# Kernel tuning notes

Measured on AMD Instinct MI355X. Metric: run time of the kernel, lower is better.

## Reference

```python
import jax, jax.numpy as jnp
import numpy as np

B, T, D, H = 2048, 2048, 3, 32  # batch, time steps, input_size, hidden_size


def setup_inputs() -> dict:
    key = jax.random.key(0)
    k0, k1, k2, k3, k4 = jax.random.split(key, 5)
    lim = 1.0 / np.sqrt(H)  # eqx.nn.GRUCell init range
    inp = jax.random.normal(k0, (B, T, D), dtype=jnp.float32)
    weight_ih = jax.random.uniform(k1, (3 * H, D), minval=-lim, maxval=lim, dtype=jnp.float32)
    weight_hh = jax.random.uniform(k2, (3 * H, H), minval=-lim, maxval=lim, dtype=jnp.float32)
    bias = jax.random.uniform(k3, (3 * H,), minval=-lim, maxval=lim, dtype=jnp.float32)
    bias_n = jax.random.uniform(k4, (H,), minval=-lim, maxval=lim, dtype=jnp.float32)
    return {"inp": inp, "weight_ih": weight_ih, "weight_hh": weight_hh,
            "bias": bias, "bias_n": bias_n}


def reference(inp, weight_ih, weight_hh, bias, bias_n):
    # inp: [B, T, D]. Faithful batched version of PinnWithGRU.__call__:
    # scan an eqx.nn.GRUCell over time from a zero hidden state, output hidden[0] per step.
    b = inp.shape[0]
    h0 = jnp.zeros((b, H), dtype=inp.dtype)
    xs = jnp.swapaxes(inp, 0, 1)  # [T, B, D]

    def step(h, x):
        ig = x @ weight_ih.T + bias      # [B, 3H] input gates (+ bias, as in eqx)
        hg = h @ weight_hh.T             # [B, 3H] hidden gates
        ir, iz, ia = jnp.split(ig, 3, axis=-1)
        hr, hz, ha = jnp.split(hg, 3, axis=-1)
        r = jax.nn.sigmoid(ir + hr)
        z = jax.nn.sigmoid(iz + hz)
        n = jnp.tanh(ia + bias_n + r * ha)
        h_new = (1.0 - z) * n + z * h
        return h_new, h_new[:, 0]        # emit first hidden unit per step

    _, out = jax.lax.scan(step, h0, xs)  # out: [T, B]
    return jnp.swapaxes(out, 0, 1)[..., None]  # [B, T, 1] (matches per-seq [T, 1])
```

## Files before the change

kernel.cpp:

```cpp
#include <hip/hip_runtime.h>


#define GRU_B 2048
#define GRU_T 2048
#define GRU_D 3
#define GRU_H 32
#define CHUNK 32

typedef unsigned int uint2v __attribute__((ext_vector_type(2)));

__device__ __forceinline__ float fast_sigmoid(float x) {
    float e = __expf(-x);
    return __builtin_amdgcn_rcpf(1.0f + e);
}
__device__ __forceinline__ float fast_tanh(float x) {
    float e = __expf(2.0f * x);
    return 1.0f - 2.0f * __builtin_amdgcn_rcpf(e + 1.0f);
}

#define DPPF(v, CTRL) __int_as_float(__builtin_amdgcn_update_dpp( \
    0, __float_as_int(v), (CTRL), 0xF, 0xF, false))

template<bool SEL>
__device__ __forceinline__ float swap32(float v) {
    uint2v r = __builtin_amdgcn_permlane32_swap(
        __float_as_uint(v), __float_as_uint(v), false, false);
    return __uint_as_float(SEL ? r.x : r.y);
}

template<bool SEL>
__device__ void gru_fast(
    const float* __restrict__ xp, float* __restrict__ ob,
    const float* __restrict__ w_ih, const float* __restrict__ w_hh,
    const float* __restrict__ bias, const float* __restrict__ bias_n,
    float* __restrict__ x_lds, float* __restrict__ out_stage,
    int lane, int hf, int p, int dir)
{
    const int li = lane & 15;
    const int bb = 16 * (lane >> 5);

    float wrO[16], wrX[16], wzO[16], wzX[16], wnO[16], wnX[16];
#pragma unroll
    for (int j = 0; j < 16; ++j) {
        const int kk = (li + dir * j + 16) & 15;
        const int kown = bb + kk;
        const int koth = (bb ^ 16) + kk;
        wrO[j] = w_hh[(size_t)p * GRU_H + kown];
        wrX[j] = w_hh[(size_t)p * GRU_H + koth];
        wzO[j] = w_hh[(size_t)(GRU_H + p) * GRU_H + kown];
        wzX[j] = w_hh[(size_t)(GRU_H + p) * GRU_H + koth];
        wnO[j] = w_hh[(size_t)(2 * GRU_H + p) * GRU_H + kown];
        wnX[j] = w_hh[(size_t)(2 * GRU_H + p) * GRU_H + koth];
    }
    float wir[GRU_D], wiz[GRU_D], win[GRU_D];
#pragma unroll
    for (int d = 0; d < GRU_D; ++d) {
        wir[d] = w_ih[(size_t)p * GRU_D + d];
        wiz[d] = w_ih[(size_t)(GRU_H + p) * GRU_D + d];
        win[d] = w_ih[(size_t)(2 * GRU_H + p) * GRU_D + d];
    }
    const float bR = bias[p];
    const float bZ = bias[GRU_H + p];
    const float bN = bias[2 * GRU_H + p] + bias_n[p];

    float* xw = x_lds + 96 * hf;
    const float* xr = x_lds + 96 * hf;
    float* osw = out_stage + 32 * hf;
    const bool cap = (lane & 47) == 0;

    float h = 0.0f;
    float xa = xp[p], xb = xp[32 + p], xc = xp[64 + p];

    for (int c = 0; c < GRU_T / CHUNK; ++c) {
        xw[p] = xa; xw[32 + p] = xb; xw[64 + p] = xc;
        if (c + 1 < GRU_T / CHUNK) {
            const size_t nb = (size_t)(c + 1) * (CHUNK * GRU_D);
            xa = xp[nb + p]; xb = xp[nb + 32 + p]; xc = xp[nb + 64 + p];
        }
#pragma unroll 8
        for (int s = 0; s < CHUNK; ++s) {
            const float x0 = xr[3 * s + 0];
            const float x1 = xr[3 * s + 1];
            const float x2 = xr[3 * s + 2];

            float hr_[16];
            hr_[0] = h;
            hr_[1]  = DPPF(h, 0x121); hr_[2]  = DPPF(h, 0x122);
            hr_[3]  = DPPF(h, 0x123); hr_[4]  = DPPF(h, 0x124);
            hr_[5]  = DPPF(h, 0x125); hr_[6]  = DPPF(h, 0x126);
            hr_[7]  = DPPF(h, 0x127); hr_[8]  = DPPF(h, 0x128);
            hr_[9]  = DPPF(h, 0x129); hr_[10] = DPPF(h, 0x12A);
            hr_[11] = DPPF(h, 0x12B); hr_[12] = DPPF(h, 0x12C);
            hr_[13] = DPPF(h, 0x12D); hr_[14] = DPPF(h, 0x12E);
            hr_[15] = DPPF(h, 0x12F);
            float ho_[16];
#pragma unroll
            for (int j = 0; j < 16; ++j) ho_[j] = swap32<SEL>(hr_[j]);

            const float aR = fmaf(wir[2], x2, fmaf(wir[1], x1, fmaf(wir[0], x0, bR)));
            const float aZ = fmaf(wiz[2], x2, fmaf(wiz[1], x1, fmaf(wiz[0], x0, bZ)));
            const float aN = fmaf(win[2], x2, fmaf(win[1], x1, fmaf(win[0], x0, bN)));

            float r0 = aR, r1 = 0.f, z0 = aZ, z1 = 0.f, n0 = 0.f, n1 = 0.f;
#pragma unroll
            for (int j = 0; j < 16; ++j) {
                r0 = fmaf(wrO[j], hr_[j], r0);
                r1 = fmaf(wrX[j], ho_[j], r1);
                z0 = fmaf(wzO[j], hr_[j], z0);
                z1 = fmaf(wzX[j], ho_[j], z1);
                n0 = fmaf(wnO[j], hr_[j], n0);
                n1 = fmaf(wnX[j], ho_[j], n1);
            }
            const float rg = fast_sigmoid(r0 + r1);
            const float zg = fast_sigmoid(z0 + z1);
            const float ng = fast_tanh(fmaf(rg, n0 + n1, aN));
            h = fmaf(zg, h - ng, ng);

            if (cap) osw[s] = h;
        }
        const float ov = osw[p];
        ob[c * CHUNK + p] = ov;
    }
}

__device__ void gru_lds(
    const float* __restrict__ xp, float* __restrict__ ob,
    const float* __restrict__ w_ih, const float* __restrict__ w_hh,
    const float* __restrict__ bias, const float* __restrict__ bias_n,
    float* __restrict__ x_lds, float* __restrict__ out_stage,
    float* __restrict__ h2, int lane, int hf, int p)
{
    float wr[32], wz[32], wn[32];
#pragma unroll
    for (int k = 0; k < 32; ++k) {
        wr[k] = w_hh[(size_t)p * GRU_H + k];
        wz[k] = w_hh[(size_t)(GRU_H + p) * GRU_H + k];
        wn[k] = w_hh[(size_t)(2 * GRU_H + p) * GRU_H + k];
    }
    float wir[GRU_D], wiz[GRU_D], win[GRU_D];
#pragma unroll
    for (int d = 0; d < GRU_D; ++d) {
        wir[d] = w_ih[(size_t)p * GRU_D + d];
        wiz[d] = w_ih[(size_t)(GRU_H + p) * GRU_D + d];
        win[d] = w_ih[(size_t)(2 * GRU_H + p) * GRU_D + d];
    }
    const float bR = bias[p];
    const float bZ = bias[GRU_H + p];
    const float bN = bias[2 * GRU_H + p] + bias_n[p];

    float* hw = h2 + 48 * hf + p;
    const float4* hv = (const float4*)(h2 + 48 * hf);
    float* xw = x_lds + 96 * hf;
    const float* xr = x_lds + 96 * hf;
    float* osw = out_stage + 32 * hf;
    const bool cap = (lane & 47) == 0;

    float h = 0.0f;
    *hw = 0.0f;
    float xa = xp[p], xb = xp[32 + p], xc = xp[64 + p];

    for (int c = 0; c < GRU_T / CHUNK; ++c) {
        xw[p] = xa; xw[32 + p] = xb; xw[64 + p] = xc;
        if (c + 1 < GRU_T / CHUNK) {
            const size_t nb = (size_t)(c + 1) * (CHUNK * GRU_D);
            xa = xp[nb + p]; xb = xp[nb + 32 + p]; xc = xp[nb + 64 + p];
        }
#pragma unroll 8
        for (int s = 0; s < CHUNK; ++s) {
            const float x0 = xr[3 * s + 0];
            const float x1 = xr[3 * s + 1];
            const float x2 = xr[3 * s + 2];
            float4 hk[8];
#pragma unroll
            for (int q = 0; q < 8; ++q) hk[q] = hv[q];

            const float aR = fmaf(wir[2], x2, fmaf(wir[1], x1, fmaf(wir[0], x0, bR)));
            const float aZ = fmaf(wiz[2], x2, fmaf(wiz[1], x1, fmaf(wiz[0], x0, bZ)));
            const float aN = fmaf(win[2], x2, fmaf(win[1], x1, fmaf(win[0], x0, bN)));

            float r0 = aR, r1 = 0.f, z0 = aZ, z1 = 0.f, n0 = 0.f, n1 = 0.f;
#pragma unroll
            for (int q = 0; q < 8; ++q) {
                const float4 v = hk[q];
                r0 = fmaf(wr[4*q+0], v.x, r0); r1 = fmaf(wr[4*q+1], v.y, r1);
                r0 = fmaf(wr[4*q+2], v.z, r0); r1 = fmaf(wr[4*q+3], v.w, r1);
                z0 = fmaf(wz[4*q+0], v.x, z0); z1 = fmaf(wz[4*q+1], v.y, z1);
                z0 = fmaf(wz[4*q+2], v.z, z0); z1 = fmaf(wz[4*q+3], v.w, z1);
                n0 = fmaf(wn[4*q+0], v.x, n0); n1 = fmaf(wn[4*q+1], v.y, n1);
                n0 = fmaf(wn[4*q+2], v.z, n0); n1 = fmaf(wn[4*q+3], v.w, n1);
            }
            const float rg = fast_sigmoid(r0 + r1);
            const float zg = fast_sigmoid(z0 + z1);
            const float ng = fast_tanh(fmaf(rg, n0 + n1, aN));
            h = fmaf(zg, h - ng, ng);
            if (cap) osw[s] = h;
            *hw = h;
        }
        const float ov = osw[p];
        ob[c * CHUNK + p] = ov;
    }
}

__global__ __launch_bounds__(64, 1) void gru_scan_kernel(
    const float* __restrict__ inp, const float* __restrict__ w_ih,
    const float* __restrict__ w_hh, const float* __restrict__ bias,
    const float* __restrict__ bias_n, float* __restrict__ out)
{
    __shared__ __align__(16) float x_lds[2 * CHUNK * GRU_D];
    __shared__ __align__(16) float out_stage[2 * CHUNK];
    __shared__ __align__(16) float h2[80];

    const int lane = threadIdx.x;
    const int hf   = (lane >> 4) & 1;
    const int p    = (lane & 15) + 16 * (lane >> 5);
    const size_t seq = 2 * (size_t)blockIdx.x + hf;

    const float* xp = inp + seq * (size_t)(GRU_T * GRU_D);
    float*       ob = out + seq * (size_t)GRU_T;

    int dir = 0;
    bool swapok = false, sel = false;
    {
        const int li = lane & 15;
        const int d1 = __builtin_amdgcn_update_dpp(0, li, 0x121, 0xF, 0xF, false);
        if (__ballot(d1 == ((li + 1) & 15)) == ~0ULL)       dir = 1;
        else if (__ballot(d1 == ((li + 15) & 15)) == ~0ULL) dir = -1;

        const unsigned ul = (unsigned)lane;
        uint2v q = __builtin_amdgcn_permlane32_swap(ul, ul, false, false);
        const unsigned want = ul ^ 32u;
        const bool okA = __ballot(q.x == want) == ~0ULL;
        const bool okB = __ballot(q.y == want) == ~0ULL;
        swapok = okA || okB;
        sel = okA;
    }

    if (dir != 0 && swapok) {
        if (sel) gru_fast<true >(xp, ob, w_ih, w_hh, bias, bias_n,
                                 x_lds, out_stage, lane, hf, p, dir);
        else     gru_fast<false>(xp, ob, w_ih, w_hh, bias, bias_n,
                                 x_lds, out_stage, lane, hf, p, dir);
    } else {
        gru_lds(xp, ob, w_ih, w_hh, bias, bias_n,
                x_lds, out_stage, h2, lane, hf, p);
    }
}

extern "C" void kernel_launch(void* const* d_in, const int* in_sizes, int n_in,
                              void* d_out, int out_size, void* d_ws, size_t ws_size,
                              hipStream_t stream) {
    const float* inp    = (const float*)d_in[0];
    const float* w_ih   = (const float*)d_in[1];
    const float* w_hh   = (const float*)d_in[2];
    const float* bias   = (const float*)d_in[3];
    const float* bias_n = (const float*)d_in[4];
    float* out = (float*)d_out;

    dim3 grid(GRU_B / 2);
    dim3 block(64);
    gru_scan_kernel<<<grid, block, 0, stream>>>(inp, w_ih, w_hh, bias, bias_n, out);
}
```

Before: 612.8 us.

## Cut per-step cross-lane ops and LDS traffic in the fast GRU recurrence

Swaps h across the 32-lane halves once with permlane32_swap and then applies the DPP rotations to both copies, which drops the 16 per-step swaps to one. Output capture moves from an LDS staging buffer to readlane/readfirstlane plus a per-lane register select. Next-step x values are prefetched from LDS one step ahead, the FMA accumulators are split into 12 shorter chains to shorten the dependency path, and the x tile is padded. The catch is twice as many DPP ops per step and two extra scalar readlanes on every step.

Result: no change. 601.2 us (-1.9%).

```diff
diff --git a/kernel.cpp b/kernel.cpp
--- a/kernel.cpp
+++ b/kernel.cpp
@@ -6,6 +6,7 @@
 #define GRU_D 3
 #define GRU_H 32
 #define CHUNK 32
+#define XPAD 104
 
 typedef unsigned int uint2v __attribute__((ext_vector_type(2)));
 
@@ -33,8 +34,7 @@
     const float* __restrict__ xp, float* __restrict__ ob,
     const float* __restrict__ w_ih, const float* __restrict__ w_hh,
     const float* __restrict__ bias, const float* __restrict__ bias_n,
-    float* __restrict__ x_lds, float* __restrict__ out_stage,
-    int lane, int hf, int p, int dir)
+    float* __restrict__ x_lds, int lane, int hf, int p, int dir)
 {
     const int li = lane & 15;
     const int bb = 16 * (lane >> 5);
@@ -63,10 +63,8 @@
     const float bZ = bias[GRU_H + p];
     const float bN = bias[2 * GRU_H + p] + bias_n[p];
 
-    float* xw = x_lds + 96 * hf;
-    const float* xr = x_lds + 96 * hf;
-    float* osw = out_stage + 32 * hf;
-    const bool cap = (lane & 47) == 0;
+    float* xw = x_lds + XPAD * hf;
+    const float* xr = x_lds + XPAD * hf;
 
     float h = 0.0f;
     float xa = xp[p], xb = xp[32 + p], xc = xp[64 + p];
@@ -77,49 +75,78 @@
             const size_t nb = (size_t)(c + 1) * (CHUNK * GRU_D);
             xa = xp[nb + p]; xb = xp[nb + 32 + p]; xc = xp[nb + 64 + p];
         }
+        float x0c = xr[0], x1c = xr[1], x2c = xr[2];
+        float outreg = 0.0f;
+
 #pragma unroll 8
         for (int s = 0; s < CHUNK; ++s) {
-            const float x0 = xr[3 * s + 0];
-            const float x1 = xr[3 * s + 1];
-            const float x2 = xr[3 * s + 2];
-
-            float hr_[16];
-            hr_[0] = h;
-            hr_[1]  = DPPF(h, 0x121); hr_[2]  = DPPF(h, 0x122);
-            hr_[3]  = DPPF(h, 0x123); hr_[4]  = DPPF(h, 0x124);
-            hr_[5]  = DPPF(h, 0x125); hr_[6]  = DPPF(h, 0x126);
-            hr_[7]  = DPPF(h, 0x127); hr_[8]  = DPPF(h, 0x128);
-            hr_[9]  = DPPF(h, 0x129); hr_[10] = DPPF(h, 0x12A);
-            hr_[11] = DPPF(h, 0x12B); hr_[12] = DPPF(h, 0x12C);
-            hr_[13] = DPPF(h, 0x12D); hr_[14] = DPPF(h, 0x12E);
-            hr_[15] = DPPF(h, 0x12F);
-            float ho_[16];
-#pragma unroll
-            for (int j = 0; j < 16; ++j) ho_[j] = swap32<SEL>(hr_[j]);
-
-            const float aR = fmaf(wir[2], x2, fmaf(wir[1], x1, fmaf(wir[0], x0, bR)));
-            const float aZ = fmaf(wiz[2], x2, fmaf(wiz[1], x1, fmaf(wiz[0], x0, bZ)));
-            const float aN = fmaf(win[2], x2, fmaf(win[1], x1, fmaf(win[0], x0, bN)));
-
-            float r0 = aR, r1 = 0.f, z0 = aZ, z1 = 0.f, n0 = 0.f, n1 = 0.f;
-#pragma unroll
-            for (int j = 0; j < 16; ++j) {
-                r0 = fmaf(wrO[j], hr_[j], r0);
-                r1 = fmaf(wrX[j], ho_[j], r1);
-                z0 = fmaf(wzO[j], hr_[j], z0);
-                z1 = fmaf(wzX[j], ho_[j], z1);
-                n0 = fmaf(wnO[j], hr_[j], n0);
-                n1 = fmaf(wnX[j], ho_[j], n1);
+            const float aR = fmaf(wir[2], x2c, fmaf(wir[1], x1c, fmaf(wir[0], x0c, bR)));
+            const float aZ = fmaf(wiz[2], x2c, fmaf(wiz[1], x1c, fmaf(wiz[0], x0c, bZ)));
+            const float aN = fmaf(win[2], x2c, fmaf(win[1], x1c, fmaf(win[0], x0c, bN)));
+
+            float x0n = x0c, x1n = x1c, x2n = x2c;
+            if (s + 1 < CHUNK) {
+                x0n = xr[3 * (s + 1) + 0];
+                x1n = xr[3 * (s + 1) + 1];
+                x2n = xr[3 * (s + 1) + 2];
             }
-            const float rg = fast_sigmoid(r0 + r1);
-            const float zg = fast_sigmoid(z0 + z1);
-            const float ng = fast_tanh(fmaf(rg, n0 + n1, aN));
+
+            const float hsw = swap32<SEL>(h);
+            float hr_[16], ho_[16];
+            hr_[0] = h;    ho_[0] = hsw;
+            hr_[1]  = DPPF(h, 0x121);   ho_[1]  = DPPF(hsw, 0x121);
+            hr_[2]  = DPPF(h, 0x122);   ho_[2]  = DPPF(hsw, 0x122);
+            hr_[3]  = DPPF(h, 0x123);   ho_[3]  = DPPF(hsw, 0x123);
+            hr_[4]  = DPPF(h, 0x124);   ho_[4]  = DPPF(hsw, 0x124);
+            hr_[5]  = DPPF(h, 0x125);   ho_[5]  = DPPF(hsw, 0x125);
+            hr_[6]  = DPPF(h, 0x126);   ho_[6]  = DPPF(hsw, 0x126);
+            hr_[7]  = DPPF(h, 0x127);   ho_[7]  = DPPF(hsw, 0x127);
+            hr_[8]  = DPPF(h, 0x128);   ho_[8]  = DPPF(hsw, 0x128);
+            hr_[9]  = DPPF(h, 0x129);   ho_[9]  = DPPF(hsw, 0x129);
+            hr_[10] = DPPF(h, 0x12A);   ho_[10] = DPPF(hsw, 0x12A);
+            hr_[11] = DPPF(h, 0x12B);   ho_[11] = DPPF(hsw, 0x12B);
+            hr_[12] = DPPF(h, 0x12C);   ho_[12] = DPPF(hsw, 0x12C);
+            hr_[13] = DPPF(h, 0x12D);   ho_[13] = DPPF(hsw, 0x12D);
+            hr_[14] = DPPF(h, 0x12E);   ho_[14] = DPPF(hsw, 0x12E);
+            hr_[15] = DPPF(h, 0x12F);   ho_[15] = DPPF(hsw, 0x12F);
+
+            float rO0 = aR, rO1 = 0.f, rX0 = 0.f, rX1 = 0.f;
+            float zO0 = aZ, zO1 = 0.f, zX0 = 0.f, zX1 = 0.f;
+            float nO0 = 0.f, nO1 = 0.f, nX0 = 0.f, nX1 = 0.f;
+#pragma unroll
+            for (int j = 0; j < 8; ++j) {
+                rO0 = fmaf(wrO[j],     hr_[j],     rO0);
+                rO1 = fmaf(wrO[j + 8], hr_[j + 8], rO1);
+                rX0 = fmaf(wrX[j],     ho_[j],     rX0);
+                rX1 = fmaf(wrX[j + 8], ho_[j + 8], rX1);
+                zO0 = fmaf(wzO[j],     hr_[j],     zO0);
+                zO1 = fmaf(wzO[j + 8], hr_[j + 8], zO1);
+                zX0 = fmaf(wzX[j],     ho_[j],     zX0);
+                zX1 = fmaf(wzX[j + 8], ho_[j + 8], zX1);
+                nO0 = fmaf(wnO[j],     hr_[j],     nO0);
+                nO1 = fmaf(wnO[j + 8], hr_[j + 8], nO1);
+                nX0 = fmaf(wnX[j],     ho_[j],     nX0);
+                nX1 = fmaf(wnX[j + 8], ho_[j + 8], nX1);
+            }
+            const float rs = (rO0 + rO1) + (rX0 + rX1);
+            const float zs = (zO0 + zO1) + (zX0 + zX1);
+            const float ns = (nO0 + nO1) + (nX0 + nX1);
+
+            const float rg = fast_sigmoid(rs);
+            const float zg = fast_sigmoid(zs);
+            const float ng = fast_tanh(fmaf(rg, ns, aN));
             h = fmaf(zg, h - ng, ng);
 
-            if (cap) osw[s] = h;
-        }
-        const float ov = osw[p];
-        ob[c * CHUNK + p] = ov;
+            const float h0A = __uint_as_float(
+                (unsigned)__builtin_amdgcn_readfirstlane(__float_as_int(h)));
+            const float h0B = __uint_as_float(
+                (unsigned)__builtin_amdgcn_readlane(__float_as_int(h), 16));
+            const float want = hf ? h0B : h0A;
+            if (p == s) outreg = want;
+
+            x0c = x0n; x1c = x1n; x2c = x2n;
+        }
+        ob[c * CHUNK + p] = outreg;
     }
 }
 
@@ -150,8 +177,8 @@
 
     float* hw = h2 + 48 * hf + p;
     const float4* hv = (const float4*)(h2 + 48 * hf);
-    float* xw = x_lds + 96 * hf;
-    const float* xr = x_lds + 96 * hf;
+    float* xw = x_lds + XPAD * hf;
+    const float* xr = x_lds + XPAD * hf;
     float* osw = out_stage + 32 * hf;
     const bool cap = (lane & 47) == 0;
 
@@ -206,7 +233,7 @@
     const float* __restrict__ w_hh, const float* __restrict__ bias,
     const float* __restrict__ bias_n, float* __restrict__ out)
 {
-    __shared__ __align__(16) float x_lds[2 * CHUNK * GRU_D];
+    __shared__ __align__(16) float x_lds[2 * XPAD];
     __shared__ __align__(16) float out_stage[2 * CHUNK];
     __shared__ __align__(16) float h2[80];
 
@@ -237,9 +264,9 @@
 
     if (dir != 0 && swapok) {
         if (sel) gru_fast<true >(xp, ob, w_ih, w_hh, bias, bias_n,
-                                 x_lds, out_stage, lane, hf, p, dir);
+                                 x_lds, lane, hf, p, dir);
         else     gru_fast<false>(xp, ob, w_ih, w_hh, bias, bias_n,
-                                 x_lds, out_stage, lane, hf, p, dir);
+                                 x_lds, lane, hf, p, dir);
     } else {
         gru_lds(xp, ob, w_ih, w_hh, bias, bias_n,
                 x_lds, out_stage, h2, lane, hf, p);
```

## Split each sequence's hidden units across a full wavefront with cross-half reduction

Applied to the files above, without the earlier changes.

Each 64-lane wavefront now handles one sequence instead of two. Lanes are split across hidden-unit halves and K halves: each lane computes 16-term partial dot products, and the halves are summed with permlane32 swaps. The new h is redistributed with permlane16_swap or ds_bpermute. Per-lane FMA work and weight registers drop by half, so more waves fit (launch bounds raised to 2 per SIMD), at the cost of extra cross-lane shuffles on the serial recurrence path and twice as many blocks. Output capture moves to readfirstlane into registers, and x loads are prefetched one step ahead.

Result: slower. 950.1 us (+55.0%).

```diff
diff --git a/kernel.cpp b/kernel.cpp
--- a/kernel.cpp
+++ b/kernel.cpp
@@ -17,6 +17,9 @@
     float e = __expf(2.0f * x);
     return 1.0f - 2.0f * __builtin_amdgcn_rcpf(e + 1.0f);
 }
+__device__ __forceinline__ float bperm(float v, int baddr) {
+    return __int_as_float(__builtin_amdgcn_ds_bpermute(baddr, __float_as_int(v)));
+}
 
 #define DPPF(v, CTRL) __int_as_float(__builtin_amdgcn_update_dpp( \
     0, __float_as_int(v), (CTRL), 0xF, 0xF, false))
@@ -28,60 +31,76 @@
     return __uint_as_float(SEL ? r.x : r.y);
 }
 
-template<bool SEL>
+#if __has_builtin(__builtin_amdgcn_permlane16_swap)
+#define HAVE_P16 1
+#else
+#define HAVE_P16 0
+#endif
+
+template<bool SEL32, bool USE16>
 __device__ void gru_fast(
     const float* __restrict__ xp, float* __restrict__ ob,
     const float* __restrict__ w_ih, const float* __restrict__ w_hh,
     const float* __restrict__ bias, const float* __restrict__ bias_n,
-    float* __restrict__ x_lds, float* __restrict__ out_stage,
-    int lane, int hf, int p, int dir)
+    float* __restrict__ x_lds, int lane, int dir, bool sel16, int a16)
 {
-    const int li = lane & 15;
-    const int bb = 16 * (lane >> 5);
-
-    float wrO[16], wrX[16], wzO[16], wzX[16], wnO[16], wnX[16];
+    const int li   = lane & 15;
+    const int row  = lane >> 4;
+    const int ublk = row & 1;
+    const int cblk = (row ^ (row >> 1)) & 1;
+    const int u     = 16 * ublk + li;
+    const int kbase = 16 * cblk;
+    const bool c0   = (cblk == 0);
+
+    float wrr[16], wzz[16], wnn[16];
 #pragma unroll
     for (int j = 0; j < 16; ++j) {
-        const int kk = (li + dir * j + 16) & 15;
-        const int kown = bb + kk;
-        const int koth = (bb ^ 16) + kk;
-        wrO[j] = w_hh[(size_t)p * GRU_H + kown];
-        wrX[j] = w_hh[(size_t)p * GRU_H + koth];
-        wzO[j] = w_hh[(size_t)(GRU_H + p) * GRU_H + kown];
-        wzX[j] = w_hh[(size_t)(GRU_H + p) * GRU_H + koth];
-        wnO[j] = w_hh[(size_t)(2 * GRU_H + p) * GRU_H + kown];
-        wnX[j] = w_hh[(size_t)(2 * GRU_H + p) * GRU_H + koth];
+        const int kk = kbase + ((li + dir * j + 16) & 15);
+        wrr[j] = w_hh[(size_t)u * GRU_H + kk];
+        wzz[j] = w_hh[(size_t)(GRU_H + u) * GRU_H + kk];
+        wnn[j] = w_hh[(size_t)(2 * GRU_H + u) * GRU_H + kk];
     }
     float wir[GRU_D], wiz[GRU_D], win[GRU_D];
 #pragma unroll
     for (int d = 0; d < GRU_D; ++d) {
-        wir[d] = w_ih[(size_t)p * GRU_D + d];
-        wiz[d] = w_ih[(size_t)(GRU_H + p) * GRU_D + d];
-        win[d] = w_ih[(size_t)(2 * GRU_H + p) * GRU_D + d];
-    }
-    const float bR = bias[p];
-    const float bZ = bias[GRU_H + p];
-    const float bN = bias[2 * GRU_H + p] + bias_n[p];
-
-    float* xw = x_lds + 96 * hf;
-    const float* xr = x_lds + 96 * hf;
-    float* osw = out_stage + 32 * hf;
-    const bool cap = (lane & 47) == 0;
+        wir[d] = c0 ? w_ih[(size_t)u * GRU_D + d] : 0.0f;
+        wiz[d] = c0 ? w_ih[(size_t)(GRU_H + u) * GRU_D + d] : 0.0f;
+        win[d] = w_ih[(size_t)(2 * GRU_H + u) * GRU_D + d];
+    }
+    const float bR = c0 ? bias[u] : 0.0f;
+    const float bZ = c0 ? bias[GRU_H + u] : 0.0f;
+    const float bN = bias[2 * GRU_H + u] + bias_n[u];
 
     float h = 0.0f;
-    float xa = xp[p], xb = xp[32 + p], xc = xp[64 + p];
+    float xr0 = xp[lane];
+    float xr1 = (lane < 32) ? xp[64 + lane] : 0.0f;
 
     for (int c = 0; c < GRU_T / CHUNK; ++c) {
-        xw[p] = xa; xw[32 + p] = xb; xw[64 + p] = xc;
+        x_lds[lane] = xr0;
+        if (lane < 32) x_lds[64 + lane] = xr1;
         if (c + 1 < GRU_T / CHUNK) {
             const size_t nb = (size_t)(c + 1) * (CHUNK * GRU_D);
-            xa = xp[nb + p]; xb = xp[nb + 32 + p]; xc = xp[nb + 64 + p];
-        }
+            xr0 = xp[nb + lane];
+            xr1 = (lane < 32) ? xp[nb + 64 + lane] : 0.0f;
+        }
+        float x0c = x_lds[0], x1c = x_lds[1], x2c = x_lds[2];
+        float outreg = 0.0f;
+
 #pragma unroll 8
         for (int s = 0; s < CHUNK; ++s) {
-            const float x0 = xr[3 * s + 0];
-            const float x1 = xr[3 * s + 1];
-            const float x2 = xr[3 * s + 2];
+            const float aR = fmaf(wir[2], x2c, fmaf(wir[1], x1c, fmaf(wir[0], x0c, bR)));
+            const float aZ = fmaf(wiz[2], x2c, fmaf(wiz[1], x1c, fmaf(wiz[0], x0c, bZ)));
+            const float aN = fmaf(win[2], x2c, fmaf(win[1], x1c, fmaf(win[0], x0c, bN)));
+
+            float x0n = x0c, x1n = x1c, x2n = x2c;
+            if (s + 1 < CHUNK) {
+                x0n = x_lds[3 * (s + 1) + 0];
+                x1n = x_lds[3 * (s + 1) + 1];
+                x2n = x_lds[3 * (s + 1) + 2];
+            }
+
+            const float hx = swap32<SEL32>(h);
+            const float hprev = (lane & 32) ? hx : h;
 
             float hr_[16];
             hr_[0] = h;
@@ -93,43 +112,60 @@
             hr_[11] = DPPF(h, 0x12B); hr_[12] = DPPF(h, 0x12C);
             hr_[13] = DPPF(h, 0x12D); hr_[14] = DPPF(h, 0x12E);
             hr_[15] = DPPF(h, 0x12F);
-            float ho_[16];
-#pragma unroll
-            for (int j = 0; j < 16; ++j) ho_[j] = swap32<SEL>(hr_[j]);
-
-            const float aR = fmaf(wir[2], x2, fmaf(wir[1], x1, fmaf(wir[0], x0, bR)));
-            const float aZ = fmaf(wiz[2], x2, fmaf(wiz[1], x1, fmaf(wiz[0], x0, bZ)));
-            const float aN = fmaf(win[2], x2, fmaf(win[1], x1, fmaf(win[0], x0, bN)));
 
             float r0 = aR, r1 = 0.f, z0 = aZ, z1 = 0.f, n0 = 0.f, n1 = 0.f;
 #pragma unroll
-            for (int j = 0; j < 16; ++j) {
-                r0 = fmaf(wrO[j], hr_[j], r0);
-                r1 = fmaf(wrX[j], ho_[j], r1);
-                z0 = fmaf(wzO[j], hr_[j], z0);
-                z1 = fmaf(wzX[j], ho_[j], z1);
-                n0 = fmaf(wnO[j], hr_[j], n0);
-                n1 = fmaf(wnX[j], ho_[j], n1);
+            for (int j = 0; j < 8; ++j) {
+                r0 = fmaf(wrr[j],     hr_[j],     r0);
+                r1 = fmaf(wrr[j + 8], hr_[j + 8], r1);
+                z0 = fmaf(wzz[j],     hr_[j],     z0);
+                z1 = fmaf(wzz[j + 8], hr_[j + 8], z1);
+                n0 = fmaf(wnn[j],     hr_[j],     n0);
+                n1 = fmaf(wnn[j + 8], hr_[j + 8], n1);
             }
-            const float rg = fast_sigmoid(r0 + r1);
-            const float zg = fast_sigmoid(z0 + z1);
-            const float ng = fast_tanh(fmaf(rg, n0 + n1, aN));
-            h = fmaf(zg, h - ng, ng);
-
-            if (cap) osw[s] = h;
-        }
-        const float ov = osw[p];
-        ob[c * CHUNK + p] = ov;
-    }
-}
-
-__device__ void gru_lds(
+            const float rh = r0 + r1;
+            const float zh = z0 + z1;
+            const float nh = n0 + n1;
+            const float rs = rh + swap32<SEL32>(rh);
+            const float zs = zh + swap32<SEL32>(zh);
+            const float ns = nh + swap32<SEL32>(nh);
+
+            const float rg = fast_sigmoid(rs);
+            const float zg = fast_sigmoid(zs);
+            const float ng = fast_tanh(fmaf(rg, ns, aN));
+            const float hnew = fmaf(zg, hprev - ng, ng);
+
+            const float h0 = __uint_as_float(
+                (unsigned)__builtin_amdgcn_readfirstlane(__float_as_int(hnew)));
+            if (lane == s) outreg = h0;
+
+            float fv;
+            if constexpr (USE16) {
+#if HAVE_P16
+                uint2v f = __builtin_amdgcn_permlane16_swap(
+                    __float_as_uint(hnew), __float_as_uint(hnew), false, false);
+                fv = __uint_as_float(sel16 ? f.x : f.y);
+#else
+                fv = bperm(hnew, a16);
+#endif
+            } else {
+                fv = bperm(hnew, a16);
+            }
+            h = (lane & 32) ? fv : hnew;
+
+            x0c = x0n; x1c = x1n; x2c = x2n;
+        }
+        if (lane < CHUNK) ob[c * CHUNK + lane] = outreg;
+    }
+}
+
+__device__ void gru_simple(
     const float* __restrict__ xp, float* __restrict__ ob,
     const float* __restrict__ w_ih, const float* __restrict__ w_hh,
     const float* __restrict__ bias, const float* __restrict__ bias_n,
-    float* __restrict__ x_lds, float* __restrict__ out_stage,
-    float* __restrict__ h2, int lane, int hf, int p)
+    float* __restrict__ x_lds, float* __restrict__ h2, int lane)
 {
+    const int p = lane & 31;
     float wr[32], wz[32], wn[32];
 #pragma unroll
     for (int k = 0; k < 32; ++k) {
@@ -148,29 +184,29 @@
     const float bZ = bias[GRU_H + p];
     const float bN = bias[2 * GRU_H + p] + bias_n[p];
 
-    float* hw = h2 + 48 * hf + p;
-    const float4* hv = (const float4*)(h2 + 48 * hf);
-    float* xw = x_lds + 96 * hf;
-    const float* xr = x_lds + 96 * hf;
-    float* osw = out_stage + 32 * hf;
-    const bool cap = (lane & 47) == 0;
-
     float h = 0.0f;
-    *hw = 0.0f;
-    float xa = xp[p], xb = xp[32 + p], xc = xp[64 + p];
+    if (lane < 32) h2[lane] = 0.0f;
+    __builtin_amdgcn_s_waitcnt(0xC07F);
+
+    float xr0 = xp[lane];
+    float xr1 = (lane < 32) ? xp[64 + lane] : 0.0f;
 
     for (int c = 0; c < GRU_T / CHUNK; ++c) {
-        xw[p] = xa; xw[32 + p] = xb; xw[64 + p] = xc;
+        x_lds[lane] = xr0;
+        if (lane < 32) x_lds[64 + lane] = xr1;
         if (c + 1 < GRU_T / CHUNK) {
             const size_t nb = (size_t)(c + 1) * (CHUNK * GRU_D);
-            xa = xp[nb + p]; xb = xp[nb + 32 + p]; xc = xp[nb + 64 + p];
-        }
-#pragma unroll 8
+            xr0 = xp[nb + lane];
+            xr1 = (lane < 32) ? xp[nb + 64 + lane] : 0.0f;
+        }
+        float outreg = 0.0f;
+#pragma unroll 4
         for (int s = 0; s < CHUNK; ++s) {
-            const float x0 = xr[3 * s + 0];
-            const float x1 = xr[3 * s + 1];
-            const float x2 = xr[3 * s + 2];
+            const float x0 = x_lds[3 * s + 0];
+            const float x1 = x_lds[3 * s + 1];
+            const float x2 = x_lds[3 * s + 2];
             float4 hk[8];
+            const float4* hv = (const float4*)h2;
 #pragma unroll
             for (int q = 0; q < 8; ++q) hk[q] = hv[q];
 
@@ -178,48 +214,48 @@
             const float aZ = fmaf(wiz[2], x2, fmaf(wiz[1], x1, fmaf(wiz[0], x0, bZ)));
             const float aN = fmaf(win[2], x2, fmaf(win[1], x1, fmaf(win[0], x0, bN)));
 
-            float r0 = aR, r1 = 0.f, z0 = aZ, z1 = 0.f, n0 = 0.f, n1 = 0.f;
+            float r0 = aR, z0 = aZ, n0 = 0.f;
 #pragma unroll
             for (int q = 0; q < 8; ++q) {
                 const float4 v = hk[q];
-                r0 = fmaf(wr[4*q+0], v.x, r0); r1 = fmaf(wr[4*q+1], v.y, r1);
-                r0 = fmaf(wr[4*q+2], v.z, r0); r1 = fmaf(wr[4*q+3], v.w, r1);
-                z0 = fmaf(wz[4*q+0], v.x, z0); z1 = fmaf(wz[4*q+1], v.y, z1);
-                z0 = fmaf(wz[4*q+2], v.z, z0); z1 = fmaf(wz[4*q+3], v.w, z1);
-                n0 = fmaf(wn[4*q+0], v.x, n0); n1 = fmaf(wn[4*q+1], v.y, n1);
-                n0 = fmaf(wn[4*q+2], v.z, n0); n1 = fmaf(wn[4*q+3], v.w, n1);
+                r0 = fmaf(wr[4*q+0], v.x, r0); r0 = fmaf(wr[4*q+1], v.y, r0);
+                r0 = fmaf(wr[4*q+2], v.z, r0); r0 = fmaf(wr[4*q+3], v.w, r0);
+                z0 = fmaf(wz[4*q+0], v.x, z0); z0 = fmaf(wz[4*q+1], v.y, z0);
+                z0 = fmaf(wz[4*q+2], v.z, z0); z0 = fmaf(wz[4*q+3], v.w, z0);
+                n0 = fmaf(wn[4*q+0], v.x, n0); n0 = fmaf(wn[4*q+1], v.y, n0);
+                n0 = fmaf(wn[4*q+2], v.z, n0); n0 = fmaf(wn[4*q+3], v.w, n0);
             }
-            const float rg = fast_sigmoid(r0 + r1);
-            const float zg = fast_sigmoid(z0 + z1);
-            const float ng = fast_tanh(fmaf(rg, n0 + n1, aN));
-            h = fmaf(zg, h - ng, ng);
-            if (cap) osw[s] = h;
-            *hw = h;
-        }
-        const float ov = osw[p];
-        ob[c * CHUNK + p] = ov;
-    }
-}
-
-__global__ __launch_bounds__(64, 1) void gru_scan_kernel(
+            const float rg = fast_sigmoid(r0);
+            const float zg = fast_sigmoid(z0);
+            const float ng = fast_tanh(fmaf(rg, n0, aN));
+            const float hnew = fmaf(zg, h - ng, ng);
+            const float h0 = __uint_as_float(
+                (unsigned)__builtin_amdgcn_readfirstlane(__float_as_int(hnew)));
+            if (lane == s) outreg = h0;
+            h = hnew;
+            if (lane < 32) h2[lane] = h;
+        }
+        if (lane < CHUNK) ob[c * CHUNK + lane] = outreg;
+    }
+}
+
+__global__ __launch_bounds__(64, 2) void gru_scan_kernel(
     const float* __restrict__ inp, const float* __restrict__ w_ih,
     const float* __restrict__ w_hh, const float* __restrict__ bias,
     const float* __restrict__ bias_n, float* __restrict__ out)
 {
-    __shared__ __align__(16) float x_lds[2 * CHUNK * GRU_D];
-    __shared__ __align__(16) float out_stage[2 * CHUNK];
-    __shared__ __align__(16) float h2[80];
+    __shared__ __align__(16) float x_lds[CHUNK * GRU_D];
+    __shared__ __align__(16) float h2[GRU_H];
 
     const int lane = threadIdx.x;
-    const int hf   = (lane >> 4) & 1;
-    const int p    = (lane & 15) + 16 * (lane >> 5);
-    const size_t seq = 2 * (size_t)blockIdx.x + hf;
+    const size_t seq = blockIdx.x;
 
     const float* xp = inp + seq * (size_t)(GRU_T * GRU_D);
     float*       ob = out + seq * (size_t)GRU_T;
+    const int a16 = (lane ^ 16) << 2;
 
     int dir = 0;
-    bool swapok = false, sel = false;
+    bool ok32 = false, sel32 = false, ok16 = false, sel16 = false;
     {
         const int li = lane & 15;
         const int d1 = __builtin_amdgcn_update_dpp(0, li, 0x121, 0xF, 0xF, false);
@@ -228,21 +264,34 @@
 
         const unsigned ul = (unsigned)lane;
         uint2v q = __builtin_amdgcn_permlane32_swap(ul, ul, false, false);
-        const unsigned want = ul ^ 32u;
-        const bool okA = __ballot(q.x == want) == ~0ULL;
-        const bool okB = __ballot(q.y == want) == ~0ULL;
-        swapok = okA || okB;
-        sel = okA;
-    }
-
-    if (dir != 0 && swapok) {
-        if (sel) gru_fast<true >(xp, ob, w_ih, w_hh, bias, bias_n,
-                                 x_lds, out_stage, lane, hf, p, dir);
-        else     gru_fast<false>(xp, ob, w_ih, w_hh, bias, bias_n,
-                                 x_lds, out_stage, lane, hf, p, dir);
+        const unsigned w32 = ul ^ 32u;
+        const bool a = __ballot(q.x == w32) == ~0ULL;
+        const bool b = __ballot(q.y == w32) == ~0ULL;
+        ok32 = a || b; sel32 = a;
+
+#if HAVE_P16
+        uint2v q16 = __builtin_amdgcn_permlane16_swap(ul, ul, false, false);
+        const unsigned w16 = ul ^ 16u;
+        const bool a16ok = __ballot(q16.x == w16) == ~0ULL;
+        const bool b16ok = __ballot(q16.y == w16) == ~0ULL;
+        ok16 = a16ok || b16ok; sel16 = a16ok;
+#endif
+    }
+
+    if (dir != 0 && ok32) {
+        if (ok16) {
+            if (sel32) gru_fast<true,  true >(xp, ob, w_ih, w_hh, bias, bias_n,
+                                              x_lds, lane, dir, sel16, a16);
+            else       gru_fast<false, true >(xp, ob, w_ih, w_hh, bias, bias_n,
+                                              x_lds, lane, dir, sel16, a16);
+        } else {
+            if (sel32) gru_fast<true,  false>(xp, ob, w_ih, w_hh, bias, bias_n,
+                                              x_lds, lane, dir, sel16, a16);
+            else       gru_fast<false, false>(xp, ob, w_ih, w_hh, bias, bias_n,
+                                              x_lds, lane, dir, sel16, a16);
+        }
     } else {
-        gru_lds(xp, ob, w_ih, w_hh, bias, bias_n,
-                x_lds, out_stage, h2, lane, hf, p);
+        gru_simple(xp, ob, w_ih, w_hh, bias, bias_n, x_lds, h2, lane);
     }
 }
 
@@ -256,7 +305,7 @@
     const float* bias_n = (const float*)d_in[4];
     float* out = (float*)d_out;
 
-    dim3 grid(GRU_B / 2);
+    dim3 grid(GRU_B);
     dim3 block(64);
     gru_scan_kernel<<<grid, block, 0, stream>>>(inp, w_ih, w_hh, bias, bias_n, out);
 }
```
